# Optimization experiments

Measured on AMD Instinct MI355X. Metric: run time of the kernel, lower is better.

## Reference

```python
import jax, jax.numpy as jnp
import numpy as np

TAU = 2.0        # LIF membrane time constant
V_TH = 1.0       # spike threshold
SG_ALPHA = 2.0   # ATan surrogate alpha (spikingjelly default)


@jax.custom_vjp
def atan_spike(x):
    # Heaviside(x) with ATan surrogate gradient
    return (x >= 0.0).astype(x.dtype)

def _atan_fwd(x):
    return atan_spike(x), x

def _atan_bwd(x, g):
    grad = (SG_ALPHA / 2.0) / (1.0 + (jnp.pi / 2.0 * SG_ALPHA * x) ** 2)
    return (g * grad,)

atan_spike.defvjp(_atan_fwd, _atan_bwd)


def lif_step(v, i_in):
    # spikingjelly LIFNode, decay_input=True, v_reset=0 (hard reset), detach_reset=True
    v = v + (i_in - v) / TAU
    s = atan_spike(v - V_TH)
    v = v * (1.0 - jax.lax.stop_gradient(s))
    return v, s


def setup_inputs() -> dict:
    key = jax.random.key(0)
    ks = jax.random.split(key, 12)
    B, C, T, M = 1024, 1, 100, 120
    D_in, H, D_out = 120, 512, 12

    def lin(kw, kb, fan_in, shape_w, shape_b):
        bound = 1.0 / np.sqrt(fan_in)
        W = jax.random.uniform(kw, shape_w, jnp.float32, -bound, bound)
        b = jax.random.uniform(kb, shape_b, jnp.float32, -bound, bound)
        return W, b

    W1, b1 = lin(ks[0], ks[1], D_in, (D_in, H), (H,))
    W2, b2 = lin(ks[2], ks[3], H, (H, H), (H,))
    W3, b3 = lin(ks[4], ks[5], H, (H, H), (H,))
    Wr, br = lin(ks[6], ks[7], H, (H, D_out), (D_out,))
    tau_m = jax.random.uniform(ks[8], (D_out,), jnp.float32, 2.0, 6.0)
    x = jax.random.normal(ks[9], (B, C, T, M), jnp.float32)
    return {"x": x, "W1": W1, "b1": b1, "W2": W2, "b2": b2,
            "W3": W3, "b3": b3, "Wr": Wr, "br": br, "tau_m": tau_m}


def reference(x, W1, b1, W2, b2, W3, b3, Wr, br, tau_m):
    B, C, T, M = x.shape
    # (B,C,T,M) -> (T,B,C*M)
    xs = jnp.transpose(x, (2, 0, 1, 3)).reshape(T, B, C * M)
    H = W1.shape[1]
    D_out = Wr.shape[1]
    alpha = jax.nn.sigmoid(tau_m)  # readout leak per output neuron

    def step(carry, xt):
        v1, v2, v3, mem = carry
        v1, s1 = lif_step(v1, xt @ W1 + b1)
        v2, s2 = lif_step(v2, s1 @ W2 + b2)
        v3, s3 = lif_step(v3, s2 @ W3 + b3)
        mem = mem * alpha + (1.0 - alpha) * (s3 @ Wr + br)
        return (v1, v2, v3, mem), mem

    z = jnp.zeros((B, H), x.dtype)
    carry0 = (z, z, z, jnp.zeros((B, D_out), x.dtype))
    _, outs = jax.lax.scan(step, carry0, xs)  # (T, B, D_out)
    logits = outs.mean(axis=0)
    return jax.nn.log_softmax(logits, axis=1)
```

## Files before the change

kernel.cpp:

```cpp
#include <hip/hip_runtime.h>
#include <cstdint>
#include <cstddef>
#include <cmath>

using u16 = unsigned short;
using u8  = unsigned char;
using s8  = signed char;
typedef float f32x4 __attribute__((ext_vector_type(4)));
typedef __bf16 bf16x8 __attribute__((ext_vector_type(8)));
typedef int i32x4 __attribute__((ext_vector_type(4)));

constexpr int BB = 1024;
constexpr int TT = 100;
constexpr int MMIN = 120;
constexpr int HH = 512;
constexpr int DD = 12;
constexpr int SEGL = 5;
constexpr int NSEG = TT / SEGL;

__device__ __forceinline__ u16 f2bf_rne(float x) {
  unsigned u = __float_as_uint(x);
  unsigned r = (u + 0x7FFFu + ((u >> 16) & 1u)) >> 16;
  return (u16)r;
}
__device__ __forceinline__ float bf2f(u16 u) {
  return __uint_as_float(((unsigned)u) << 16);
}

__global__ __launch_bounds__(256) void wsplit_kernel(
    const float* __restrict__ W, u16* __restrict__ Thi, u16* __restrict__ Tlo,
    int K, int N, int kp_shift) {
  int gid = blockIdx.x * 256 + threadIdx.x;
  int KP = 1 << kp_shift;
  int k = gid & (KP - 1);
  int n = gid >> kp_shift;
  float v = 0.0f;
  if (k < K && n < N) v = W[(size_t)k * N + n];
  u16 hi = f2bf_rne(v);
  Thi[gid] = hi;
  Tlo[gid] = f2bf_rne(v - bf2f(hi));
}

__global__ __launch_bounds__(256) void wquant_kernel(
    const float* __restrict__ W, s8* __restrict__ T1, s8* __restrict__ T2,
    int N, float s1, float inv1, float s2) {
  int gid = blockIdx.x * 256 + threadIdx.x;
  int k = gid & 511;
  int n = gid >> 9;
  float v = (n < N) ? W[(size_t)k * N + n] : 0.0f;
  int q1 = (int)rintf(v * s1);
  q1 = q1 > 127 ? 127 : (q1 < -127 ? -127 : q1);
  float r1 = v - (float)q1 * inv1;
  int q2 = (int)rintf(r1 * s2);
  q2 = q2 > 127 ? 127 : (q2 < -127 ? -127 : q2);
  T1[gid] = (s8)q1;
  T2[gid] = (s8)q2;
}

__global__ __launch_bounds__(256) void xsplit_kernel(
    const float* __restrict__ x, u16* __restrict__ xhi, u16* __restrict__ xlo, int t0) {
  int gid = blockIdx.x * 256 + threadIdx.x;
  int m = gid & 127;
  int r = gid >> 7;
  int b = r & (BB - 1);
  int t = t0 + (r >> 10);
  float v = 0.0f;
  if (m < MMIN) v = x[(size_t)b * (TT * MMIN) + (size_t)t * MMIN + m];
  u16 hi = f2bf_rne(v);
  xhi[gid] = hi;
  xlo[gid] = f2bf_rne(v - bf2f(hi));
}

typedef const __attribute__((address_space(1))) unsigned int gas_uint;
typedef __attribute__((address_space(3))) unsigned int las_uint;

__device__ __forceinline__ void gl_lds16(const void* g, void* l) {
  __builtin_amdgcn_global_load_lds((gas_uint*)g, (las_uint*)l, 16, 0, 0);
}

__global__ __launch_bounds__(256, 2) void fusedq(
    const u8* __restrict__ Sin, const s8* __restrict__ T1,
    const s8* __restrict__ T2, const float* __restrict__ bias,
    float* __restrict__ vstate, u8* __restrict__ Sout,
    int TC, int firstc, float inv2) {
  __shared__ __align__(16) u8 lds[4][8192];

  const int x = blockIdx.x;
  const int hh = (x >> 3) & 7;
  const int bb = ((x >> 6) << 3) | (x & 7);
  const int tid = threadIdx.x;
  const int wv = tid >> 6, lane = tid & 63;
  const int lr = lane & 15, lg = lane >> 4;
  const int habs = hh * 64 + wv * 16;
  const int babs = bb * 16;

  i32x4 Wd1[8], Wd2[8];
#pragma unroll
  for (int ks = 0; ks < 8; ++ks) {
    size_t o = (size_t)(habs + lr) * 512 + ks * 64 + lg * 16;
    Wd1[ks] = *(const i32x4*)(T1 + o);
    Wd2[ks] = *(const i32x4*)(T2 + o);
  }

  float bi[4], v[4];
#pragma unroll
  for (int j = 0; j < 4; ++j) {
    int h = habs + lg * 4 + j;
    bi[j] = bias[h];
    v[j] = firstc ? 0.0f : vstate[(size_t)(babs + lr) * 512 + h];
  }

  const u8* gs[2]; int dso[2];
#pragma unroll
  for (int p = 0; p < 2; ++p) {
    int li = p * 256 + tid;
    int r = li >> 5, c = li & 31;
    int cs = c ^ (r & 7);
    gs[p] = Sin + (size_t)(babs + r) * 512 + cs * 16;
    dso[p] = (li & ~63) * 16;
  }
  auto stage = [&](int taddr, int bufi) {
    u8* b = &lds[bufi][0];
    size_t o = (size_t)taddr * 524288;
    gl_lds16(gs[0] + o, b + dso[0]);
    gl_lds16(gs[1] + o, b + dso[1]);
  };

  u8* obase = Sout + (size_t)(babs + lr) * 512 + habs + lg * 4;
  const int sm = lr & 7;

  i32x4 s[2][8];
  stage(0, 0); stage(1, 1); stage(2, 2);
  asm volatile("s_waitcnt vmcnt(2)" ::: "memory");
  __builtin_amdgcn_sched_barrier(0);
  __builtin_amdgcn_s_barrier();
  __builtin_amdgcn_sched_barrier(0);
  {
    const u8* sb = &lds[0][0];
#pragma unroll
    for (int ks = 0; ks < 8; ++ks)
      s[0][ks] = *(const i32x4*)&sb[lr * 512 + (((ks * 4 + lg) ^ sm) << 4)];
  }

#define FQ_BODY(T_, PC_)                                                       \
  do {                                                                         \
    asm volatile("s_waitcnt vmcnt(2)" ::: "memory");                           \
    __builtin_amdgcn_sched_barrier(0);                                         \
    __builtin_amdgcn_s_barrier();                                              \
    __builtin_amdgcn_sched_barrier(0);                                         \
    int t3_ = (T_) + 3; if (t3_ >= TC) t3_ -= TC;                              \
    stage(t3_, ((T_) + 3) & 3);                                                \
    const u8* sb_ = &lds[((T_) + 1) & 3][0];                                   \
    _Pragma("unroll")                                                          \
    for (int ks = 0; ks < 8; ++ks)                                             \
      s[PC_ ^ 1][ks] = *(const i32x4*)&sb_[lr * 512 + (((ks * 4 + lg) ^ sm) << 4)]; \
    __builtin_amdgcn_sched_barrier(0);                                         \
    i32x4 p0_ = (i32x4)0, p1_ = (i32x4)0, q0_ = (i32x4)0, q1_ = (i32x4)0;      \
    _Pragma("unroll")                                                          \
    for (int ks = 0; ks < 4; ++ks) {                                           \
      p0_ = __builtin_amdgcn_mfma_i32_16x16x64_i8(Wd1[ks], s[PC_][ks], p0_, 0, 0, 0);          \
      q0_ = __builtin_amdgcn_mfma_i32_16x16x64_i8(Wd2[ks], s[PC_][ks], q0_, 0, 0, 0);          \
      p1_ = __builtin_amdgcn_mfma_i32_16x16x64_i8(Wd1[ks + 4], s[PC_][ks + 4], p1_, 0, 0, 0);  \
      q1_ = __builtin_amdgcn_mfma_i32_16x16x64_i8(Wd2[ks + 4], s[PC_][ks + 4], q1_, 0, 0, 0);  \
    }                                                                          \
    unsigned w_ = 0;                                                           \
    _Pragma("unroll")                                                          \
    for (int j = 0; j < 4; ++j) {                                              \
      int A1_ = p0_[j] + p1_[j];                                               \
      int A2_ = q0_[j] + q1_[j];                                               \
      float I_ = (float)(A1_ * 254 + A2_) * inv2 + bi[j];                      \
      float vv_ = v[j] + (I_ - v[j]) * 0.5f;                                   \
      int spk_ = vv_ >= 1.0f;                                                  \
      v[j] = spk_ ? 0.0f : vv_;                                                \
      w_ |= (unsigned)spk_ << (8 * j);                                         \
    }                                                                          \
    *(unsigned*)(obase + (size_t)(T_) * 524288) = w_;                          \
  } while (0)

  for (int t = 0; t + 1 < TC; t += 2) {
    FQ_BODY(t, 0);
    FQ_BODY(t + 1, 1);
  }
#undef FQ_BODY
  asm volatile("s_waitcnt vmcnt(0)" ::: "memory");

#pragma unroll
  for (int j = 0; j < 4; ++j)
    vstate[(size_t)(babs + lr) * 512 + habs + lg * 4 + j] = v[j];
}

__global__ __launch_bounds__(256, 2) void fused1(
    const u16* __restrict__ xh, const u16* __restrict__ xl,
    const u16* __restrict__ Th, const u16* __restrict__ Tl,
    const float* __restrict__ bias, float* __restrict__ vstate,
    u8* __restrict__ Sout, int TC, int firstc) {
  __shared__ __align__(16) u8 lds[4][8192];

  const int x = blockIdx.x;
  const int hh = (x >> 3) & 7;
  const int bb = ((x >> 6) << 3) | (x & 7);
  const int tid = threadIdx.x;
  const int wv = tid >> 6, lane = tid & 63;
  const int lr = lane & 15, lg = lane >> 4;
  const int habs = hh * 64 + wv * 16;
  const int babs = bb * 16;

  bf16x8 Wh[4], Wl[4];
#pragma unroll
  for (int ks = 0; ks < 4; ++ks) {
    size_t o = (size_t)(habs + lr) * 128 + ks * 32 + lg * 8;
    Wh[ks] = *(const bf16x8*)(Th + o);
    Wl[ks] = *(const bf16x8*)(Tl + o);
  }

  float bi[4], v[4];
#pragma unroll
  for (int j = 0; j < 4; ++j) {
    int h = habs + lg * 4 + j;
    bi[j] = bias[h];
    v[j] = firstc ? 0.0f : vstate[(size_t)(babs + lr) * 512 + h];
  }

  const u16* gs[2]; int dso[2];
#pragma unroll
  for (int p = 0; p < 2; ++p) {
    int li = p * 256 + tid;
    const u16* src = (li < 256) ? xh : xl;
    int lj = li & 255;
    int r = lj >> 4, c = lj & 15;
    int cs = c ^ (r & 7);
    gs[p] = src + (size_t)(babs + r) * 128 + cs * 8;
    dso[p] = (li & ~63) * 16;
  }
  auto stage = [&](int taddr, int bufi) {
    u8* b = &lds[bufi][0];
    size_t o = (size_t)taddr * 131072;
    gl_lds16(gs[0] + o, b + dso[0]);
    gl_lds16(gs[1] + o, b + dso[1]);
  };

  u8* obase = Sout + (size_t)(babs + lr) * 512 + habs + lg * 4;
  const int sm = lr & 7;

  bf16x8 s[2][8];
  stage(0, 0); stage(1, 1); stage(2, 2);
  asm volatile("s_waitcnt vmcnt(2)" ::: "memory");
  __builtin_amdgcn_sched_barrier(0);
  __builtin_amdgcn_s_barrier();
  __builtin_amdgcn_sched_barrier(0);
  {
    const u8* sb = &lds[0][0];
#pragma unroll
    for (int ks = 0; ks < 4; ++ks) {
      int co = ((ks * 4 + lg) ^ sm) << 4;
      s[0][ks] = *(const bf16x8*)&sb[lr * 256 + co];
      s[0][4 + ks] = *(const bf16x8*)&sb[4096 + lr * 256 + co];
    }
  }

#define F1_BODY(T_, PC_)                                                       \
  do {                                                                         \
    asm volatile("s_waitcnt vmcnt(2)" ::: "memory");                           \
    __builtin_amdgcn_sched_barrier(0);                                         \
    __builtin_amdgcn_s_barrier();                                              \
    __builtin_amdgcn_sched_barrier(0);                                         \
    int t3_ = (T_) + 3; if (t3_ >= TC) t3_ -= TC;                              \
    stage(t3_, ((T_) + 3) & 3);                                                \
    const u8* sb_ = &lds[((T_) + 1) & 3][0];                                   \
    _Pragma("unroll")                                                          \
    for (int ks = 0; ks < 4; ++ks) {                                           \
      int co_ = ((ks * 4 + lg) ^ sm) << 4;                                     \
      s[PC_ ^ 1][ks] = *(const bf16x8*)&sb_[lr * 256 + co_];                   \
      s[PC_ ^ 1][4 + ks] = *(const bf16x8*)&sb_[4096 + lr * 256 + co_];        \
    }                                                                          \
    __builtin_amdgcn_sched_barrier(0);                                         \
    f32x4 aa_ = (f32x4)0.0f, ab_ = (f32x4)0.0f, ac_ = (f32x4)0.0f;             \
    _Pragma("unroll")                                                          \
    for (int ks = 0; ks < 4; ++ks) {                                           \
      aa_ = __builtin_amdgcn_mfma_f32_16x16x32_bf16(Wh[ks], s[PC_][ks], aa_, 0, 0, 0);     \
      ab_ = __builtin_amdgcn_mfma_f32_16x16x32_bf16(Wl[ks], s[PC_][ks], ab_, 0, 0, 0);     \
      ac_ = __builtin_amdgcn_mfma_f32_16x16x32_bf16(Wh[ks], s[PC_][4 + ks], ac_, 0, 0, 0); \
    }                                                                          \
    unsigned w_ = 0;                                                           \
    _Pragma("unroll")                                                          \
    for (int j = 0; j < 4; ++j) {                                              \
      float I_ = aa_[j] + ab_[j] + ac_[j] + bi[j];                             \
      float vv_ = v[j] + (I_ - v[j]) * 0.5f;                                   \
      int spk_ = vv_ >= 1.0f;                                                  \
      v[j] = spk_ ? 0.0f : vv_;                                                \
      w_ |= (unsigned)spk_ << (8 * j);                                         \
    }                                                                          \
    *(unsigned*)(obase + (size_t)(T_) * 524288) = w_;                          \
  } while (0)

  for (int t = 0; t + 1 < TC; t += 2) {
    F1_BODY(t, 0);
    F1_BODY(t + 1, 1);
  }
#undef F1_BODY
  asm volatile("s_waitcnt vmcnt(0)" ::: "memory");

#pragma unroll
  for (int j = 0; j < 4; ++j)
    vstate[(size_t)(babs + lr) * 512 + habs + lg * 4 + j] = v[j];
}

__global__ __launch_bounds__(256) void readout_kernel(
    const u8* __restrict__ S, const s8* __restrict__ T1,
    const s8* __restrict__ T2, float* __restrict__ R,
    float inv1, float inv2) {
  const int wv = threadIdx.x >> 6, lane = threadIdx.x & 63;
  const int lr = lane & 15, lg = lane >> 4;
  const int row0 = blockIdx.x * 256 + wv * 64;
  const s8* b1 = T1 + (size_t)lr * 512 + lg * 16;
  const s8* b2 = T2 + (size_t)lr * 512 + lg * 16;
#pragma unroll
  for (int sub = 0; sub < 4; ++sub) {
    i32x4 acc1 = (i32x4)0, acc2 = (i32x4)0;
    const u8* arow = S + (size_t)(row0 + sub * 16 + lr) * 512 + lg * 16;
#pragma unroll
    for (int kt = 0; kt < 8; ++kt) {
      i32x4 a  = *(const i32x4*)(arow + kt * 64);
      i32x4 h1 = *(const i32x4*)(b1 + kt * 64);
      i32x4 h2 = *(const i32x4*)(b2 + kt * 64);
      acc1 = __builtin_amdgcn_mfma_i32_16x16x64_i8(a, h1, acc1, 0, 0, 0);
      acc2 = __builtin_amdgcn_mfma_i32_16x16x64_i8(a, h2, acc2, 0, 0, 0);
    }
#pragma unroll
    for (int j = 0; j < 4; ++j)
      R[(size_t)(row0 + sub * 16 + lg * 4 + j) * 16 + lr] =
          (float)acc1[j] * inv1 + (float)acc2[j] * inv2;
  }
}

__global__ __launch_bounds__(256) void memseg_kernel(
    const float* __restrict__ R, const float* __restrict__ br,
    const float* __restrict__ tau, float* __restrict__ qbuf,
    float* __restrict__ sbuf, int t0) {
  int gid = blockIdx.x * 256 + threadIdx.x;
  int b = gid & 1023;
  int sg = gid >> 10;
  float al[DD], bb[DD], m[DD], s[DD];
#pragma unroll
  for (int d = 0; d < DD; ++d) {
    al[d] = 1.0f / (1.0f + expf(-tau[d]));
    bb[d] = br[d];
    m[d] = 0.0f; s[d] = 0.0f;
  }
  for (int i = 0; i < SEGL; ++i) {
    int t = sg * SEGL + i;
    const float4* q = (const float4*)(R + ((size_t)t * BB + b) * 16);
    float4 q0 = q[0], q1 = q[1], q2 = q[2];
    float r[DD] = {q0.x, q0.y, q0.z, q0.w, q1.x, q1.y, q1.z, q1.w, q2.x, q2.y, q2.z, q2.w};
#pragma unroll
    for (int d = 0; d < DD; ++d) {
      float rv = r[d] + bb[d];
      m[d] = m[d] * al[d] + (1.0f - al[d]) * rv;
      s[d] += m[d];
    }
  }
  int gseg = t0 / SEGL + sg;
#pragma unroll
  for (int d = 0; d < DD; ++d) {
    qbuf[((size_t)gseg * BB + b) * DD + d] = m[d];
    sbuf[((size_t)gseg * BB + b) * DD + d] = s[d];
  }
}

__global__ __launch_bounds__(256) void memcombine_kernel(
    const float* __restrict__ qbuf, const float* __restrict__ sbuf,
    const float* __restrict__ tau, float* __restrict__ out) {
  int b = blockIdx.x * 256 + threadIdx.x;
  float al[DD], pL[DD], geo[DD], mem[DD], sum[DD];
#pragma unroll
  for (int d = 0; d < DD; ++d) {
    al[d] = 1.0f / (1.0f + expf(-tau[d]));
    float pl = 1.0f, g = 0.0f;
#pragma unroll
    for (int j = 0; j < SEGL; ++j) { pl *= al[d]; g += pl; }
    pL[d] = pl; geo[d] = g;
    mem[d] = 0.0f; sum[d] = 0.0f;
  }
  for (int g = 0; g < NSEG; ++g) {
    size_t o = ((size_t)g * BB + b) * DD;
#pragma unroll
    for (int d = 0; d < DD; ++d) {
      sum[d] += sbuf[o + d] + geo[d] * mem[d];
      mem[d] = pL[d] * mem[d] + qbuf[o + d];
    }
  }
  float l[DD];
#pragma unroll
  for (int d = 0; d < DD; ++d) l[d] = sum[d] * (1.0f / (float)TT);
  float mx = l[0];
#pragma unroll
  for (int d = 1; d < DD; ++d) mx = fmaxf(mx, l[d]);
  float se = 0.0f;
#pragma unroll
  for (int d = 0; d < DD; ++d) se += expf(l[d] - mx);
  float lse = logf(se);
#pragma unroll
  for (int d = 0; d < DD; ++d) out[b * DD + d] = l[d] - mx - lse;
}

extern "C" void kernel_launch(void* const* d_in, const int* in_sizes, int n_in,
                              void* d_out, int out_size, void* d_ws, size_t ws_size,
                              hipStream_t stream) {
  (void)in_sizes; (void)n_in; (void)out_size;
  const float* x   = (const float*)d_in[0];
  const float* W1  = (const float*)d_in[1];
  const float* b1  = (const float*)d_in[2];
  const float* W2  = (const float*)d_in[3];
  const float* b2  = (const float*)d_in[4];
  const float* W3  = (const float*)d_in[5];
  const float* b3  = (const float*)d_in[6];
  const float* Wr  = (const float*)d_in[7];
  const float* br  = (const float*)d_in[8];
  const float* tau = (const float*)d_in[9];
  float* out = (float*)d_out;

  const double s1d = 127.0 * 22.627416997969522;
  const double s2d = 254.0 * s1d;
  const float s1 = (float)s1d, inv1 = (float)(1.0 / s1d);
  const float s2 = (float)s2d, inv2 = (float)(1.0 / s2d);

  const size_t fixed_bytes = (size_t)12 << 20;
  const size_t per_tc = (size_t)(524288 + 524288 + 524288 + 65536 + 4096);
  int TC = 10;
  const int cands[4] = {100, 50, 20, 10};
  for (int i = 0; i < 4; ++i) {
    if (fixed_bytes + (size_t)cands[i] * per_tc <= ws_size) { TC = cands[i]; break; }
  }

  char* base = (char*)d_ws;
  size_t off = 0;
  auto alloc = [&](size_t bytes) -> char* {
    char* p = base + off;
    off += (bytes + 255) & ~(size_t)255;
    return p;
  };

  u16* W1Th = (u16*)alloc(512 * 128 * 2);
  u16* W1Tl = (u16*)alloc(512 * 128 * 2);
  s8* W2q1 = (s8*)alloc(512 * 512);
  s8* W2q2 = (s8*)alloc(512 * 512);
  s8* W3q1 = (s8*)alloc(512 * 512);
  s8* W3q2 = (s8*)alloc(512 * 512);
  s8* Wrq1 = (s8*)alloc(16 * 512);
  s8* Wrq2 = (s8*)alloc(16 * 512);
  float* v1 = (float*)alloc((size_t)BB * HH * 4);
  float* v2 = (float*)alloc((size_t)BB * HH * 4);
  float* v3 = (float*)alloc((size_t)BB * HH * 4);
  float* qbuf = (float*)alloc((size_t)NSEG * BB * DD * 4);
  float* sbuf = (float*)alloc((size_t)NSEG * BB * DD * 4);
  u16* xh = (u16*)alloc((size_t)TC * BB * 128 * 2 * 2);
  u16* xl = xh + (size_t)TC * BB * 128;
  u8*  S3 = (u8*)xh;
  u8*  S1 = (u8*)alloc((size_t)TC * BB * HH);
  u8*  S2 = (u8*)alloc((size_t)TC * BB * HH);
  float* Rbuf = (float*)alloc((size_t)TC * BB * 16 * 4);

  wsplit_kernel<<<dim3((512 * 128) / 256), dim3(256), 0, stream>>>(W1, W1Th, W1Tl, 120, 512, 7);
  wquant_kernel<<<dim3((512 * 512) / 256), dim3(256), 0, stream>>>(W2, W2q1, W2q2, 512, s1, inv1, s2);
  wquant_kernel<<<dim3((512 * 512) / 256), dim3(256), 0, stream>>>(W3, W3q1, W3q2, 512, s1, inv1, s2);
  wquant_kernel<<<dim3((16 * 512) / 256), dim3(256), 0, stream>>>(Wr, Wrq1, Wrq2, 12, s1, inv1, s2);

  const int NC = TT / TC;
  for (int c = 0; c < NC; ++c) {
    int t0 = c * TC;
    int Mc = TC * BB;
    int first = (c == 0) ? 1 : 0;
    xsplit_kernel<<<dim3(TC * 512), dim3(256), 0, stream>>>(x, xh, xl, t0);
    fused1<<<dim3(512), dim3(256), 0, stream>>>(xh, xl, W1Th, W1Tl, b1, v1, S1, TC, first);
    fusedq<<<dim3(512), dim3(256), 0, stream>>>(S1, W2q1, W2q2, b2, v2, S2, TC, first, inv2);
    fusedq<<<dim3(512), dim3(256), 0, stream>>>(S2, W3q1, W3q2, b3, v3, S3, TC, first, inv2);
    readout_kernel<<<dim3(Mc / 256), dim3(256), 0, stream>>>(S3, Wrq1, Wrq2, Rbuf, inv1, inv2);
    memseg_kernel<<<dim3((TC / SEGL) * 4), dim3(256), 0, stream>>>(
        Rbuf, br, tau, qbuf, sbuf, t0);
  }
  memcombine_kernel<<<dim3(4), dim3(256), 0, stream>>>(qbuf, sbuf, tau, out);
}
```

Measured before the change: 248.5 us.

## Halve waves per block so each wave computes two 16-row hidden fragments

The fused LIF layer kernels now launch 128 threads (2 waves) per block instead of 256, with each wave handling 32 hidden units (two MFMA M-fragments) against the same staged spike tile. Each spike fragment read from LDS is reused across two weight fragments. Staging issues 4 loads per thread, and the vmcnt waits are adjusted to match. In exchange, each wave holds twice the weight registers, and launch bounds drop to 1 block per CU, which cuts total resident waves and may reduce latency hiding.

```diff
diff --git a/kernel.cpp b/kernel.cpp
--- a/kernel.cpp
+++ b/kernel.cpp
@@ -78,7 +78,7 @@
   __builtin_amdgcn_global_load_lds((gas_uint*)g, (las_uint*)l, 16, 0, 0);
 }
 
-__global__ __launch_bounds__(256, 2) void fusedq(
+__global__ __launch_bounds__(128, 1) void fusedq(
     const u8* __restrict__ Sin, const s8* __restrict__ T1,
     const s8* __restrict__ T2, const float* __restrict__ bias,
     float* __restrict__ vstate, u8* __restrict__ Sout,
@@ -91,29 +91,33 @@
   const int tid = threadIdx.x;
   const int wv = tid >> 6, lane = tid & 63;
   const int lr = lane & 15, lg = lane >> 4;
-  const int habs = hh * 64 + wv * 16;
+  const int habs = hh * 64 + wv * 32;
   const int babs = bb * 16;
 
-  i32x4 Wd1[8], Wd2[8];
-#pragma unroll
-  for (int ks = 0; ks < 8; ++ks) {
-    size_t o = (size_t)(habs + lr) * 512 + ks * 64 + lg * 16;
-    Wd1[ks] = *(const i32x4*)(T1 + o);
-    Wd2[ks] = *(const i32x4*)(T2 + o);
-  }
-
-  float bi[4], v[4];
-#pragma unroll
-  for (int j = 0; j < 4; ++j) {
-    int h = habs + lg * 4 + j;
-    bi[j] = bias[h];
-    v[j] = firstc ? 0.0f : vstate[(size_t)(babs + lr) * 512 + h];
-  }
-
-  const u8* gs[2]; int dso[2];
-#pragma unroll
-  for (int p = 0; p < 2; ++p) {
-    int li = p * 256 + tid;
+  i32x4 Wd1[2][8], Wd2[2][8];
+#pragma unroll
+  for (int mf = 0; mf < 2; ++mf)
+#pragma unroll
+    for (int ks = 0; ks < 8; ++ks) {
+      size_t o = (size_t)(habs + mf * 16 + lr) * 512 + ks * 64 + lg * 16;
+      Wd1[mf][ks] = *(const i32x4*)(T1 + o);
+      Wd2[mf][ks] = *(const i32x4*)(T2 + o);
+    }
+
+  float bi[2][4], v[2][4];
+#pragma unroll
+  for (int mf = 0; mf < 2; ++mf)
+#pragma unroll
+    for (int j = 0; j < 4; ++j) {
+      int h = habs + mf * 16 + lg * 4 + j;
+      bi[mf][j] = bias[h];
+      v[mf][j] = firstc ? 0.0f : vstate[(size_t)(babs + lr) * 512 + h];
+    }
+
+  const u8* gs[4]; int dso[4];
+#pragma unroll
+  for (int p = 0; p < 4; ++p) {
+    int li = p * 128 + tid;
     int r = li >> 5, c = li & 31;
     int cs = c ^ (r & 7);
     gs[p] = Sin + (size_t)(babs + r) * 512 + cs * 16;
@@ -124,6 +128,8 @@
     size_t o = (size_t)taddr * 524288;
     gl_lds16(gs[0] + o, b + dso[0]);
     gl_lds16(gs[1] + o, b + dso[1]);
+    gl_lds16(gs[2] + o, b + dso[2]);
+    gl_lds16(gs[3] + o, b + dso[3]);
   };
 
   u8* obase = Sout + (size_t)(babs + lr) * 512 + habs + lg * 4;
@@ -131,7 +137,7 @@
 
   i32x4 s[2][8];
   stage(0, 0); stage(1, 1); stage(2, 2);
-  asm volatile("s_waitcnt vmcnt(2)" ::: "memory");
+  asm volatile("s_waitcnt vmcnt(4)" ::: "memory");
   __builtin_amdgcn_sched_barrier(0);
   __builtin_amdgcn_s_barrier();
   __builtin_amdgcn_sched_barrier(0);
@@ -144,7 +150,7 @@
 
 #define FQ_BODY(T_, PC_)                                                       \
   do {                                                                         \
-    asm volatile("s_waitcnt vmcnt(2)" ::: "memory");                           \
+    asm volatile("s_waitcnt vmcnt(6)" ::: "memory");                           \
     __builtin_amdgcn_sched_barrier(0);                                         \
     __builtin_amdgcn_s_barrier();                                              \
     __builtin_amdgcn_sched_barrier(0);                                         \
@@ -155,26 +161,29 @@
     for (int ks = 0; ks < 8; ++ks)                                             \
       s[PC_ ^ 1][ks] = *(const i32x4*)&sb_[lr * 512 + (((ks * 4 + lg) ^ sm) << 4)]; \
     __builtin_amdgcn_sched_barrier(0);                                         \
-    i32x4 p0_ = (i32x4)0, p1_ = (i32x4)0, q0_ = (i32x4)0, q1_ = (i32x4)0;      \
     _Pragma("unroll")                                                          \
-    for (int ks = 0; ks < 4; ++ks) {                                           \
-      p0_ = __builtin_amdgcn_mfma_i32_16x16x64_i8(Wd1[ks], s[PC_][ks], p0_, 0, 0, 0);          \
-      q0_ = __builtin_amdgcn_mfma_i32_16x16x64_i8(Wd2[ks], s[PC_][ks], q0_, 0, 0, 0);          \
-      p1_ = __builtin_amdgcn_mfma_i32_16x16x64_i8(Wd1[ks + 4], s[PC_][ks + 4], p1_, 0, 0, 0);  \
-      q1_ = __builtin_amdgcn_mfma_i32_16x16x64_i8(Wd2[ks + 4], s[PC_][ks + 4], q1_, 0, 0, 0);  \
+    for (int mf = 0; mf < 2; ++mf) {                                           \
+      i32x4 p0_ = (i32x4)0, p1_ = (i32x4)0, q0_ = (i32x4)0, q1_ = (i32x4)0;    \
+      _Pragma("unroll")                                                        \
+      for (int ks = 0; ks < 4; ++ks) {                                         \
+        p0_ = __builtin_amdgcn_mfma_i32_16x16x64_i8(Wd1[mf][ks], s[PC_][ks], p0_, 0, 0, 0);         \
+        q0_ = __builtin_amdgcn_mfma_i32_16x16x64_i8(Wd2[mf][ks], s[PC_][ks], q0_, 0, 0, 0);         \
+        p1_ = __builtin_amdgcn_mfma_i32_16x16x64_i8(Wd1[mf][ks + 4], s[PC_][ks + 4], p1_, 0, 0, 0); \
+        q1_ = __builtin_amdgcn_mfma_i32_16x16x64_i8(Wd2[mf][ks + 4], s[PC_][ks + 4], q1_, 0, 0, 0); \
+      }                                                                        \
+      unsigned w_ = 0;                                                         \
+      _Pragma("unroll")                                                        \
+      for (int j = 0; j < 4; ++j) {                                            \
+        int A1_ = p0_[j] + p1_[j];                                             \
+        int A2_ = q0_[j] + q1_[j];                                             \
+        float I_ = (float)(A1_ * 254 + A2_) * inv2 + bi[mf][j];                \
+        float vv_ = v[mf][j] + (I_ - v[mf][j]) * 0.5f;                         \
+        int spk_ = vv_ >= 1.0f;                                                \
+        v[mf][j] = spk_ ? 0.0f : vv_;                                          \
+        w_ |= (unsigned)spk_ << (8 * j);                                       \
+      }                                                                        \
+      *(unsigned*)(obase + (size_t)(T_) * 524288 + mf * 16) = w_;              \
     }                                                                          \
-    unsigned w_ = 0;                                                           \
-    _Pragma("unroll")                                                          \
-    for (int j = 0; j < 4; ++j) {                                              \
-      int A1_ = p0_[j] + p1_[j];                                               \
-      int A2_ = q0_[j] + q1_[j];                                               \
-      float I_ = (float)(A1_ * 254 + A2_) * inv2 + bi[j];                      \
-      float vv_ = v[j] + (I_ - v[j]) * 0.5f;                                   \
-      int spk_ = vv_ >= 1.0f;                                                  \
-      v[j] = spk_ ? 0.0f : vv_;                                                \
-      w_ |= (unsigned)spk_ << (8 * j);                                         \
-    }                                                                          \
-    *(unsigned*)(obase + (size_t)(T_) * 524288) = w_;                          \
   } while (0)
 
   for (int t = 0; t + 1 < TC; t += 2) {
@@ -185,11 +194,13 @@
   asm volatile("s_waitcnt vmcnt(0)" ::: "memory");
 
 #pragma unroll
-  for (int j = 0; j < 4; ++j)
-    vstate[(size_t)(babs + lr) * 512 + habs + lg * 4 + j] = v[j];
-}
-
-__global__ __launch_bounds__(256, 2) void fused1(
+  for (int mf = 0; mf < 2; ++mf)
+#pragma unroll
+    for (int j = 0; j < 4; ++j)
+      vstate[(size_t)(babs + lr) * 512 + habs + mf * 16 + lg * 4 + j] = v[mf][j];
+}
+
+__global__ __launch_bounds__(128, 1) void fused1(
     const u16* __restrict__ xh, const u16* __restrict__ xl,
     const u16* __restrict__ Th, const u16* __restrict__ Tl,
     const float* __restrict__ bias, float* __restrict__ vstate,
@@ -202,41 +213,46 @@
   const int tid = threadIdx.x;
   const int wv = tid >> 6, lane = tid & 63;
   const int lr = lane & 15, lg = lane >> 4;
-  const int habs = hh * 64 + wv * 16;
+  const int habs = hh * 64 + wv * 32;
   const int babs = bb * 16;
 
-  bf16x8 Wh[4], Wl[4];
-#pragma unroll
-  for (int ks = 0; ks < 4; ++ks) {
-    size_t o = (size_t)(habs + lr) * 128 + ks * 32 + lg * 8;
-    Wh[ks] = *(const bf16x8*)(Th + o);
-    Wl[ks] = *(const bf16x8*)(Tl + o);
-  }
-
-  float bi[4], v[4];
-#pragma unroll
-  for (int j = 0; j < 4; ++j) {
-    int h = habs + lg * 4 + j;
-    bi[j] = bias[h];
-    v[j] = firstc ? 0.0f : vstate[(size_t)(babs + lr) * 512 + h];
-  }
-
-  const u16* gs[2]; int dso[2];
-#pragma unroll
-  for (int p = 0; p < 2; ++p) {
-    int li = p * 256 + tid;
-    const u16* src = (li < 256) ? xh : xl;
-    int lj = li & 255;
+  bf16x8 Wh[2][4], Wl[2][4];
+#pragma unroll
+  for (int mf = 0; mf < 2; ++mf)
+#pragma unroll
+    for (int ks = 0; ks < 4; ++ks) {
+      size_t o = (size_t)(habs + mf * 16 + lr) * 128 + ks * 32 + lg * 8;
+      Wh[mf][ks] = *(const bf16x8*)(Th + o);
+      Wl[mf][ks] = *(const bf16x8*)(Tl + o);
+    }
+
+  float bi[2][4], v[2][4];
+#pragma unroll
+  for (int mf = 0; mf < 2; ++mf)
+#pragma unroll
+    for (int j = 0; j < 4; ++j) {
+      int h = habs + mf * 16 + lg * 4 + j;
+      bi[mf][j] = bias[h];
+      v[mf][j] = firstc ? 0.0f : vstate[(size_t)(babs + lr) * 512 + h];
+    }
+
+  const u16* gs[4]; int dso[4];
+#pragma unroll
+  for (int p = 0; p < 4; ++p) {
+    int lj = (p & 1) * 128 + tid;
     int r = lj >> 4, c = lj & 15;
     int cs = c ^ (r & 7);
+    const u16* src = (p < 2) ? xh : xl;
     gs[p] = src + (size_t)(babs + r) * 128 + cs * 8;
-    dso[p] = (li & ~63) * 16;
+    dso[p] = ((p < 2) ? 0 : 4096) + (lj & ~63) * 16;
   }
   auto stage = [&](int taddr, int bufi) {
     u8* b = &lds[bufi][0];
     size_t o = (size_t)taddr * 131072;
     gl_lds16(gs[0] + o, b + dso[0]);
     gl_lds16(gs[1] + o, b + dso[1]);
+    gl_lds16(gs[2] + o, b + dso[2]);
+    gl_lds16(gs[3] + o, b + dso[3]);
   };
 
   u8* obase = Sout + (size_t)(babs + lr) * 512 + habs + lg * 4;
@@ -244,7 +260,7 @@
 
   bf16x8 s[2][8];
   stage(0, 0); stage(1, 1); stage(2, 2);
-  asm volatile("s_waitcnt vmcnt(2)" ::: "memory");
+  asm volatile("s_waitcnt vmcnt(4)" ::: "memory");
   __builtin_amdgcn_sched_barrier(0);
   __builtin_amdgcn_s_barrier();
   __builtin_amdgcn_sched_barrier(0);
@@ -260,7 +276,7 @@
 
 #define F1_BODY(T_, PC_)                                                       \
   do {                                                                         \
-    asm volatile("s_waitcnt vmcnt(2)" ::: "memory");                           \
+    asm volatile("s_waitcnt vmcnt(6)" ::: "memory");                           \
     __builtin_amdgcn_sched_barrier(0);                                         \
     __builtin_amdgcn_s_barrier();                                              \
     __builtin_amdgcn_sched_barrier(0);                                         \
@@ -274,23 +290,26 @@
       s[PC_ ^ 1][4 + ks] = *(const bf16x8*)&sb_[4096 + lr * 256 + co_];        \
     }                                                                          \
     __builtin_amdgcn_sched_barrier(0);                                         \
-    f32x4 aa_ = (f32x4)0.0f, ab_ = (f32x4)0.0f, ac_ = (f32x4)0.0f;             \
     _Pragma("unroll")                                                          \
-    for (int ks = 0; ks < 4; ++ks) {                                           \
-      aa_ = __builtin_amdgcn_mfma_f32_16x16x32_bf16(Wh[ks], s[PC_][ks], aa_, 0, 0, 0);     \
-      ab_ = __builtin_amdgcn_mfma_f32_16x16x32_bf16(Wl[ks], s[PC_][ks], ab_, 0, 0, 0);     \
-      ac_ = __builtin_amdgcn_mfma_f32_16x16x32_bf16(Wh[ks], s[PC_][4 + ks], ac_, 0, 0, 0); \
+    for (int mf = 0; mf < 2; ++mf) {                                           \
+      f32x4 aa_ = (f32x4)0.0f, ab_ = (f32x4)0.0f, ac_ = (f32x4)0.0f;           \
+      _Pragma("unroll")                                                        \
+      for (int ks = 0; ks < 4; ++ks) {                                         \
+        aa_ = __builtin_amdgcn_mfma_f32_16x16x32_bf16(Wh[mf][ks], s[PC_][ks], aa_, 0, 0, 0);     \
+        ab_ = __builtin_amdgcn_mfma_f32_16x16x32_bf16(Wl[mf][ks], s[PC_][ks], ab_, 0, 0, 0);     \
+        ac_ = __builtin_amdgcn_mfma_f32_16x16x32_bf16(Wh[mf][ks], s[PC_][4 + ks], ac_, 0, 0, 0); \
+      }                                                                        \
+      unsigned w_ = 0;                                                         \
+      _Pragma("unroll")                                                        \
+      for (int j = 0; j < 4; ++j) {                                            \
+        float I_ = aa_[j] + ab_[j] + ac_[j] + bi[mf][j];                       \
+        float vv_ = v[mf][j] + (I_ - v[mf][j]) * 0.5f;                         \
+        int spk_ = vv_ >= 1.0f;                                                \
+        v[mf][j] = spk_ ? 0.0f : vv_;                                          \
+        w_ |= (unsigned)spk_ << (8 * j);                                       \
+      }                                                                        \
+      *(unsigned*)(obase + (size_t)(T_) * 524288 + mf * 16) = w_;              \
     }                                                                          \
-    unsigned w_ = 0;                                                           \
-    _Pragma("unroll")                                                          \
-    for (int j = 0; j < 4; ++j) {                                              \
-      float I_ = aa_[j] + ab_[j] + ac_[j] + bi[j];                             \
-      float vv_ = v[j] + (I_ - v[j]) * 0.5f;                                   \
-      int spk_ = vv_ >= 1.0f;                                                  \
-      v[j] = spk_ ? 0.0f : vv_;                                                \
-      w_ |= (unsigned)spk_ << (8 * j);                                         \
-    }                                                                          \
-    *(unsigned*)(obase + (size_t)(T_) * 524288) = w_;                          \
   } while (0)
 
   for (int t = 0; t + 1 < TC; t += 2) {
@@ -301,8 +320,10 @@
   asm volatile("s_waitcnt vmcnt(0)" ::: "memory");
 
 #pragma unroll
-  for (int j = 0; j < 4; ++j)
-    vstate[(size_t)(babs + lr) * 512 + habs + lg * 4 + j] = v[j];
+  for (int mf = 0; mf < 2; ++mf)
+#pragma unroll
+    for (int j = 0; j < 4; ++j)
+      vstate[(size_t)(babs + lr) * 512 + habs + mf * 16 + lg * 4 + j] = v[mf][j];
 }
 
 __global__ __launch_bounds__(256) void readout_kernel(
@@ -471,9 +492,9 @@
     int Mc = TC * BB;
     int first = (c == 0) ? 1 : 0;
     xsplit_kernel<<<dim3(TC * 512), dim3(256), 0, stream>>>(x, xh, xl, t0);
-    fused1<<<dim3(512), dim3(256), 0, stream>>>(xh, xl, W1Th, W1Tl, b1, v1, S1, TC, first);
-    fusedq<<<dim3(512), dim3(256), 0, stream>>>(S1, W2q1, W2q2, b2, v2, S2, TC, first, inv2);
-    fusedq<<<dim3(512), dim3(256), 0, stream>>>(S2, W3q1, W3q2, b3, v3, S3, TC, first, inv2);
+    fused1<<<dim3(512), dim3(128), 0, stream>>>(xh, xl, W1Th, W1Tl, b1, v1, S1, TC, first);
+    fusedq<<<dim3(512), dim3(128), 0, stream>>>(S1, W2q1, W2q2, b2, v2, S2, TC, first, inv2);
+    fusedq<<<dim3(512), dim3(128), 0, stream>>>(S2, W3q1, W3q2, b3, v3, S3, TC, first, inv2);
     readout_kernel<<<dim3(Mc / 256), dim3(256), 0, stream>>>(S3, Wrq1, Wrq2, Rbuf, inv1, inv2);
     memseg_kernel<<<dim3((TC / SEGL) * 4), dim3(256), 0, stream>>>(
         Rbuf, br, tau, qbuf, sbuf, t0);
```

New measurement: 287.6 us. 15.7% more time.

## Deepen LDS pipeline to six buffers, process two timesteps per barrier, merge weight prep

Applied to the files above, without the earlier changes.

Both fused LIF layer kernels now use six LDS buffers instead of four and process two timesteps per barrier. Each step stages two future tiles and prefetches the next pair into registers through alternating register sets, which is meant to halve barrier count and hide more load latency. The four weight preparation kernels are merged into one launch, and the TC candidates are reduced to {100, 20}. Costs are more LDS (48KB per block) and more registers, which can reduce occupancy. TC must now be a multiple of 4.

```diff
diff --git a/kernel.cpp b/kernel.cpp
--- a/kernel.cpp
+++ b/kernel.cpp
@@ -27,10 +27,8 @@
   return __uint_as_float(((unsigned)u) << 16);
 }
 
-__global__ __launch_bounds__(256) void wsplit_kernel(
-    const float* __restrict__ W, u16* __restrict__ Thi, u16* __restrict__ Tlo,
-    int K, int N, int kp_shift) {
-  int gid = blockIdx.x * 256 + threadIdx.x;
+__device__ __forceinline__ void wsplit_body(const float* W, u16* Thi, u16* Tlo,
+                                            int gid, int K, int N, int kp_shift) {
   int KP = 1 << kp_shift;
   int k = gid & (KP - 1);
   int n = gid >> kp_shift;
@@ -40,11 +38,8 @@
   Thi[gid] = hi;
   Tlo[gid] = f2bf_rne(v - bf2f(hi));
 }
-
-__global__ __launch_bounds__(256) void wquant_kernel(
-    const float* __restrict__ W, s8* __restrict__ T1, s8* __restrict__ T2,
-    int N, float s1, float inv1, float s2) {
-  int gid = blockIdx.x * 256 + threadIdx.x;
+__device__ __forceinline__ void wquant_body(const float* W, s8* T1, s8* T2,
+                                            int gid, int N, float s1, float inv1, float s2) {
   int k = gid & 511;
   int n = gid >> 9;
   float v = (n < N) ? W[(size_t)k * N + n] : 0.0f;
@@ -55,6 +50,18 @@
   q2 = q2 > 127 ? 127 : (q2 < -127 ? -127 : q2);
   T1[gid] = (s8)q1;
   T2[gid] = (s8)q2;
+}
+__global__ __launch_bounds__(256) void wprep_kernel(
+    const float* __restrict__ W1, u16* __restrict__ W1Th, u16* __restrict__ W1Tl,
+    const float* __restrict__ W2, s8* __restrict__ W2q1, s8* __restrict__ W2q2,
+    const float* __restrict__ W3, s8* __restrict__ W3q1, s8* __restrict__ W3q2,
+    const float* __restrict__ Wr, s8* __restrict__ Wrq1, s8* __restrict__ Wrq2,
+    float s1, float inv1, float s2) {
+  int b = blockIdx.x, tid = threadIdx.x;
+  if (b < 256)       wsplit_body(W1, W1Th, W1Tl, b * 256 + tid, 120, 512, 7);
+  else if (b < 1280) wquant_body(W2, W2q1, W2q2, (b - 256) * 256 + tid, 512, s1, inv1, s2);
+  else if (b < 2304) wquant_body(W3, W3q1, W3q2, (b - 1280) * 256 + tid, 512, s1, inv1, s2);
+  else               wquant_body(Wr, Wrq1, Wrq2, (b - 2304) * 256 + tid, 12, s1, inv1, s2);
 }
 
 __global__ __launch_bounds__(256) void xsplit_kernel(
@@ -83,7 +90,7 @@
     const s8* __restrict__ T2, const float* __restrict__ bias,
     float* __restrict__ vstate, u8* __restrict__ Sout,
     int TC, int firstc, float inv2) {
-  __shared__ __align__(16) u8 lds[4][8192];
+  __shared__ __align__(16) u8 lds[6][8192];
 
   const int x = blockIdx.x;
   const int hh = (x >> 3) & 7;
@@ -125,43 +132,38 @@
     gl_lds16(gs[0] + o, b + dso[0]);
     gl_lds16(gs[1] + o, b + dso[1]);
   };
+  auto rdtile = [&](i32x4* dst, int bufi) {
+    const u8* sb = &lds[bufi][0];
+    const int sm = lr & 7;
+#pragma unroll
+    for (int ks = 0; ks < 8; ++ks)
+      dst[ks] = *(const i32x4*)&sb[lr * 512 + (((ks * 4 + lg) ^ sm) << 4)];
+  };
 
   u8* obase = Sout + (size_t)(babs + lr) * 512 + habs + lg * 4;
-  const int sm = lr & 7;
-
-  i32x4 s[2][8];
-  stage(0, 0); stage(1, 1); stage(2, 2);
-  asm volatile("s_waitcnt vmcnt(2)" ::: "memory");
+
+  i32x4 sA[2][8], sB[2][8];
+
+  stage(0, 0); stage(1, 1); stage(2, 2); stage(3, 3);
+  asm volatile("s_waitcnt vmcnt(0)" ::: "memory");
   __builtin_amdgcn_sched_barrier(0);
   __builtin_amdgcn_s_barrier();
   __builtin_amdgcn_sched_barrier(0);
-  {
-    const u8* sb = &lds[0][0];
-#pragma unroll
-    for (int ks = 0; ks < 8; ++ks)
-      s[0][ks] = *(const i32x4*)&sb[lr * 512 + (((ks * 4 + lg) ^ sm) << 4)];
-  }
-
-#define FQ_BODY(T_, PC_)                                                       \
+  rdtile(sA[0], 0);
+  rdtile(sA[1], 1);
+
+  int tb = 0;
+  int ta = 4;
+
+#define FQ_T(SREG)                                                             \
   do {                                                                         \
-    asm volatile("s_waitcnt vmcnt(2)" ::: "memory");                           \
-    __builtin_amdgcn_sched_barrier(0);                                         \
-    __builtin_amdgcn_s_barrier();                                              \
-    __builtin_amdgcn_sched_barrier(0);                                         \
-    int t3_ = (T_) + 3; if (t3_ >= TC) t3_ -= TC;                              \
-    stage(t3_, ((T_) + 3) & 3);                                                \
-    const u8* sb_ = &lds[((T_) + 1) & 3][0];                                   \
-    _Pragma("unroll")                                                          \
-    for (int ks = 0; ks < 8; ++ks)                                             \
-      s[PC_ ^ 1][ks] = *(const i32x4*)&sb_[lr * 512 + (((ks * 4 + lg) ^ sm) << 4)]; \
-    __builtin_amdgcn_sched_barrier(0);                                         \
     i32x4 p0_ = (i32x4)0, p1_ = (i32x4)0, q0_ = (i32x4)0, q1_ = (i32x4)0;      \
     _Pragma("unroll")                                                          \
     for (int ks = 0; ks < 4; ++ks) {                                           \
-      p0_ = __builtin_amdgcn_mfma_i32_16x16x64_i8(Wd1[ks], s[PC_][ks], p0_, 0, 0, 0);          \
-      q0_ = __builtin_amdgcn_mfma_i32_16x16x64_i8(Wd2[ks], s[PC_][ks], q0_, 0, 0, 0);          \
-      p1_ = __builtin_amdgcn_mfma_i32_16x16x64_i8(Wd1[ks + 4], s[PC_][ks + 4], p1_, 0, 0, 0);  \
-      q1_ = __builtin_amdgcn_mfma_i32_16x16x64_i8(Wd2[ks + 4], s[PC_][ks + 4], q1_, 0, 0, 0);  \
+      p0_ = __builtin_amdgcn_mfma_i32_16x16x64_i8(Wd1[ks], (SREG)[ks], p0_, 0, 0, 0);          \
+      q0_ = __builtin_amdgcn_mfma_i32_16x16x64_i8(Wd2[ks], (SREG)[ks], q0_, 0, 0, 0);          \
+      p1_ = __builtin_amdgcn_mfma_i32_16x16x64_i8(Wd1[ks + 4], (SREG)[ks + 4], p1_, 0, 0, 0);  \
+      q1_ = __builtin_amdgcn_mfma_i32_16x16x64_i8(Wd2[ks + 4], (SREG)[ks + 4], q1_, 0, 0, 0);  \
     }                                                                          \
     unsigned w_ = 0;                                                           \
     _Pragma("unroll")                                                          \
@@ -174,14 +176,39 @@
       v[j] = spk_ ? 0.0f : vv_;                                                \
       w_ |= (unsigned)spk_ << (8 * j);                                         \
     }                                                                          \
-    *(unsigned*)(obase + (size_t)(T_) * 524288) = w_;                          \
+    *(unsigned*)(obase + (size_t)tcur * 524288) = w_;                          \
   } while (0)
 
-  for (int t = 0; t + 1 < TC; t += 2) {
-    FQ_BODY(t, 0);
-    FQ_BODY(t + 1, 1);
-  }
-#undef FQ_BODY
+#define FQ_STEP(CUR, NXT)                                                      \
+  do {                                                                         \
+    __builtin_amdgcn_s_barrier();                                              \
+    __builtin_amdgcn_sched_barrier(0);                                         \
+    int st0 = tb + 4; if (st0 >= 6) st0 -= 6;                                  \
+    int st1 = tb + 5; if (st1 >= 6) st1 -= 6;                                  \
+    int ta1 = ta + 1;                                                          \
+    stage(ta, st0); stage(ta1, st1);                                           \
+    asm volatile("s_waitcnt vmcnt(6)" ::: "memory");                           \
+    __builtin_amdgcn_sched_barrier(0);                                         \
+    int pf0 = tb + 2; if (pf0 >= 6) pf0 -= 6;                                  \
+    int pf1 = tb + 3; if (pf1 >= 6) pf1 -= 6;                                  \
+    rdtile(NXT[0], pf0); rdtile(NXT[1], pf1);                                  \
+    __builtin_amdgcn_sched_barrier(0);                                         \
+    int tcur = t;                                                              \
+    FQ_T(CUR[0]);                                                              \
+    tcur = t + 1;                                                              \
+    FQ_T(CUR[1]);                                                              \
+    tb += 2; if (tb >= 6) tb -= 6;                                             \
+    ta += 2; if (ta >= TC) ta -= TC;                                           \
+  } while (0)
+
+  for (int t = 0; t < TC; t += 4) {
+    FQ_STEP(sA, sB);
+    t += 2;
+    FQ_STEP(sB, sA);
+    t -= 2;
+  }
+#undef FQ_STEP
+#undef FQ_T
   asm volatile("s_waitcnt vmcnt(0)" ::: "memory");
 
 #pragma unroll
@@ -194,7 +221,7 @@
     const u16* __restrict__ Th, const u16* __restrict__ Tl,
     const float* __restrict__ bias, float* __restrict__ vstate,
     u8* __restrict__ Sout, int TC, int firstc) {
-  __shared__ __align__(16) u8 lds[4][8192];
+  __shared__ __align__(16) u8 lds[6][8192];
 
   const int x = blockIdx.x;
   const int hh = (x >> 3) & 7;
@@ -238,48 +265,40 @@
     gl_lds16(gs[0] + o, b + dso[0]);
     gl_lds16(gs[1] + o, b + dso[1]);
   };
+  auto rdtile = [&](bf16x8* dst, int bufi) {
+    const u8* sb = &lds[bufi][0];
+    const int sm = lr & 7;
+#pragma unroll
+    for (int ks = 0; ks < 4; ++ks) {
+      int co = ((ks * 4 + lg) ^ sm) << 4;
+      dst[ks] = *(const bf16x8*)&sb[lr * 256 + co];
+      dst[4 + ks] = *(const bf16x8*)&sb[4096 + lr * 256 + co];
+    }
+  };
 
   u8* obase = Sout + (size_t)(babs + lr) * 512 + habs + lg * 4;
-  const int sm = lr & 7;
-
-  bf16x8 s[2][8];
-  stage(0, 0); stage(1, 1); stage(2, 2);
-  asm volatile("s_waitcnt vmcnt(2)" ::: "memory");
+
+  bf16x8 sA[2][8], sB[2][8];
+
+  stage(0, 0); stage(1, 1); stage(2, 2); stage(3, 3);
+  asm volatile("s_waitcnt vmcnt(0)" ::: "memory");
   __builtin_amdgcn_sched_barrier(0);
   __builtin_amdgcn_s_barrier();
   __builtin_amdgcn_sched_barrier(0);
-  {
-    const u8* sb = &lds[0][0];
-#pragma unroll
-    for (int ks = 0; ks < 4; ++ks) {
-      int co = ((ks * 4 + lg) ^ sm) << 4;
-      s[0][ks] = *(const bf16x8*)&sb[lr * 256 + co];
-      s[0][4 + ks] = *(const bf16x8*)&sb[4096 + lr * 256 + co];
-    }
-  }
-
-#define F1_BODY(T_, PC_)                                                       \
+  rdtile(sA[0], 0);
+  rdtile(sA[1], 1);
+
+  int tb = 0;
+  int ta = 4;
+
+#define F1_T(SREG)                                                             \
   do {                                                                         \
-    asm volatile("s_waitcnt vmcnt(2)" ::: "memory");                           \
-    __builtin_amdgcn_sched_barrier(0);                                         \
-    __builtin_amdgcn_s_barrier();                                              \
-    __builtin_amdgcn_sched_barrier(0);                                         \
-    int t3_ = (T_) + 3; if (t3_ >= TC) t3_ -= TC;                              \
-    stage(t3_, ((T_) + 3) & 3);                                                \
-    const u8* sb_ = &lds[((T_) + 1) & 3][0];                                   \
-    _Pragma("unroll")                                                          \
-    for (int ks = 0; ks < 4; ++ks) {                                           \
-      int co_ = ((ks * 4 + lg) ^ sm) << 4;                                     \
-      s[PC_ ^ 1][ks] = *(const bf16x8*)&sb_[lr * 256 + co_];                   \
-      s[PC_ ^ 1][4 + ks] = *(const bf16x8*)&sb_[4096 + lr * 256 + co_];        \
-    }                                                                          \
-    __builtin_amdgcn_sched_barrier(0);                                         \
     f32x4 aa_ = (f32x4)0.0f, ab_ = (f32x4)0.0f, ac_ = (f32x4)0.0f;             \
     _Pragma("unroll")                                                          \
     for (int ks = 0; ks < 4; ++ks) {                                           \
-      aa_ = __builtin_amdgcn_mfma_f32_16x16x32_bf16(Wh[ks], s[PC_][ks], aa_, 0, 0, 0);     \
-      ab_ = __builtin_amdgcn_mfma_f32_16x16x32_bf16(Wl[ks], s[PC_][ks], ab_, 0, 0, 0);     \
-      ac_ = __builtin_amdgcn_mfma_f32_16x16x32_bf16(Wh[ks], s[PC_][4 + ks], ac_, 0, 0, 0); \
+      aa_ = __builtin_amdgcn_mfma_f32_16x16x32_bf16(Wh[ks], (SREG)[ks], aa_, 0, 0, 0);     \
+      ab_ = __builtin_amdgcn_mfma_f32_16x16x32_bf16(Wl[ks], (SREG)[ks], ab_, 0, 0, 0);     \
+      ac_ = __builtin_amdgcn_mfma_f32_16x16x32_bf16(Wh[ks], (SREG)[4 + ks], ac_, 0, 0, 0); \
     }                                                                          \
     unsigned w_ = 0;                                                           \
     _Pragma("unroll")                                                          \
@@ -290,14 +309,39 @@
       v[j] = spk_ ? 0.0f : vv_;                                                \
       w_ |= (unsigned)spk_ << (8 * j);                                         \
     }                                                                          \
-    *(unsigned*)(obase + (size_t)(T_) * 524288) = w_;                          \
+    *(unsigned*)(obase + (size_t)tcur * 524288) = w_;                          \
   } while (0)
 
-  for (int t = 0; t + 1 < TC; t += 2) {
-    F1_BODY(t, 0);
-    F1_BODY(t + 1, 1);
-  }
-#undef F1_BODY
+#define F1_STEP(CUR, NXT)                                                      \
+  do {                                                                         \
+    __builtin_amdgcn_s_barrier();                                              \
+    __builtin_amdgcn_sched_barrier(0);                                         \
+    int st0 = tb + 4; if (st0 >= 6) st0 -= 6;                                  \
+    int st1 = tb + 5; if (st1 >= 6) st1 -= 6;                                  \
+    int ta1 = ta + 1;                                                          \
+    stage(ta, st0); stage(ta1, st1);                                           \
+    asm volatile("s_waitcnt vmcnt(6)" ::: "memory");                           \
+    __builtin_amdgcn_sched_barrier(0);                                         \
+    int pf0 = tb + 2; if (pf0 >= 6) pf0 -= 6;                                  \
+    int pf1 = tb + 3; if (pf1 >= 6) pf1 -= 6;                                  \
+    rdtile(NXT[0], pf0); rdtile(NXT[1], pf1);                                  \
+    __builtin_amdgcn_sched_barrier(0);                                         \
+    int tcur = t;                                                              \
+    F1_T(CUR[0]);                                                              \
+    tcur = t + 1;                                                              \
+    F1_T(CUR[1]);                                                              \
+    tb += 2; if (tb >= 6) tb -= 6;                                             \
+    ta += 2; if (ta >= TC) ta -= TC;                                           \
+  } while (0)
+
+  for (int t = 0; t < TC; t += 4) {
+    F1_STEP(sA, sB);
+    t += 2;
+    F1_STEP(sB, sA);
+    t -= 2;
+  }
+#undef F1_STEP
+#undef F1_T
   asm volatile("s_waitcnt vmcnt(0)" ::: "memory");
 
 #pragma unroll
@@ -426,9 +470,9 @@
 
   const size_t fixed_bytes = (size_t)12 << 20;
   const size_t per_tc = (size_t)(524288 + 524288 + 524288 + 65536 + 4096);
-  int TC = 10;
-  const int cands[4] = {100, 50, 20, 10};
-  for (int i = 0; i < 4; ++i) {
+  int TC = 20;
+  const int cands[2] = {100, 20};
+  for (int i = 0; i < 2; ++i) {
     if (fixed_bytes + (size_t)cands[i] * per_tc <= ws_size) { TC = cands[i]; break; }
   }
 
@@ -460,10 +504,9 @@
   u8*  S2 = (u8*)alloc((size_t)TC * BB * HH);
   float* Rbuf = (float*)alloc((size_t)TC * BB * 16 * 4);
 
-  wsplit_kernel<<<dim3((512 * 128) / 256), dim3(256), 0, stream>>>(W1, W1Th, W1Tl, 120, 512, 7);
-  wquant_kernel<<<dim3((512 * 512) / 256), dim3(256), 0, stream>>>(W2, W2q1, W2q2, 512, s1, inv1, s2);
-  wquant_kernel<<<dim3((512 * 512) / 256), dim3(256), 0, stream>>>(W3, W3q1, W3q2, 512, s1, inv1, s2);
-  wquant_kernel<<<dim3((16 * 512) / 256), dim3(256), 0, stream>>>(Wr, Wrq1, Wrq2, 12, s1, inv1, s2);
+  wprep_kernel<<<dim3(2336), dim3(256), 0, stream>>>(
+      W1, W1Th, W1Tl, W2, W2q1, W2q2, W3, W3q1, W3q2, Wr, Wrq1, Wrq2,
+      s1, inv1, s2);
 
   const int NC = TT / TC;
   for (int c = 0; c < NC; ++c) {
```

After: 238.8 us (median of 2 runs). 1.04x faster.
